# Kernel optimization log

Measured on AMD Instinct MI355X. Metric: run time of the kernel, lower is better.

Reference implementation:

```python
import jax, jax.numpy as jnp
import numpy as np

NUM_AGENTS = 5
B = 512          # graphs in batch
NP = 50          # nodes per graph
N = B * NP
EPG = 400        # edges per graph
E = B * EPG
H, C = 8, 64     # heads, per-head channels
F = H * C        # 512 node feature dim after concat
GRU_IN = 2 * F   # agent emb + graph emb
GRU_H = 128


def _gat_layer(x, src, dst, ea, W, a_src, a_dst, We, ae, b):
    # PyG GATConv: per-edge additive attention with edge features, softmax over dst
    n = x.shape[0]
    h = (x @ W).reshape(n, H, C)                          # [n,H,C]
    al = (h * a_src).sum(-1)[src] + (h * a_dst).sum(-1)[dst] \
         + ((ea @ We).reshape(-1, H, C) * ae).sum(-1)     # [e,H]
    al = jax.nn.leaky_relu(al, 0.2)
    amax = jax.ops.segment_max(al, dst, num_segments=n)
    amax = jnp.where(jnp.isfinite(amax), amax, 0.0)
    p = jnp.exp(al - amax[dst])
    denom = jax.ops.segment_sum(p, dst, num_segments=n)
    alpha = p / (denom[dst] + 1e-16)
    out = jax.ops.segment_sum(alpha[:, :, None] * h[src], dst, num_segments=n)
    return out.reshape(n, F) + b


def _gru(x_seq, h0, Wih, Whh, bih, bhh):
    # torch nn.GRU math, batch_first input [B,T,I]
    def step(h, x_t):
        gi = x_t @ Wih + bih
        gh = h @ Whh + bhh
        ir, iz, inn = jnp.split(gi, 3, axis=-1)
        hr, hz, hn = jnp.split(gh, 3, axis=-1)
        r = jax.nn.sigmoid(ir + hr)
        z = jax.nn.sigmoid(iz + hz)
        n_ = jnp.tanh(inn + r * hn)
        h_new = (1.0 - z) * n_ + z * h
        return h_new, h_new
    h_last, ys = jax.lax.scan(step, h0, jnp.swapaxes(x_seq, 0, 1))
    return jnp.swapaxes(ys, 0, 1), h_last


def _forward(x, edge_index, edge_attr, hidden_state,
             W1, a_src1, a_dst1, We1, ae1, b1,
             W2, a_src2, a_dst2, We2, ae2, b2,
             W3, a_src3, a_dst3, We3, ae3, b3,
             gru_Wih, gru_Whh, gru_bih, gru_bhh,
             fc1_W, fc1_b, fc2_W, fc2_b, log_std):
    src, dst = edge_index[0], edge_index[1]
    # conv1: add_self_loops=False
    x1 = jax.nn.relu(_gat_layer(x, src, dst, edge_attr, W1, a_src1, a_dst1, We1, ae1, b1))
    # conv2/3: add self loops with fill_value='mean' (mean of incoming edge_attr per node)
    cnt = jax.ops.segment_sum(jnp.ones((E,), x.dtype), dst, num_segments=N)
    loop_attr = jax.ops.segment_sum(edge_attr, dst, num_segments=N) / jnp.maximum(cnt, 1.0)[:, None]
    loops = jnp.arange(N, dtype=edge_index.dtype)
    src2 = jnp.concatenate([src, loops])
    dst2 = jnp.concatenate([dst, loops])
    ea2 = jnp.concatenate([edge_attr, loop_attr], axis=0)
    x2 = jax.nn.relu(_gat_layer(x1, src2, dst2, ea2, W2, a_src2, a_dst2, We2, ae2, b2))
    x3 = jax.nn.relu(_gat_layer(x2, src2, dst2, ea2, W3, a_src3, a_dst3, We3, ae3, b3))
    # global mean pool (each graph has NP nodes, contiguous)
    batch = jnp.repeat(jnp.arange(B), NP)
    graph_emb = jax.ops.segment_sum(x3, batch, num_segments=B) / NP   # [B,F]
    # first NUM_AGENTS nodes of each graph
    agent_idx = (jnp.arange(B)[:, None] * NP + jnp.arange(NUM_AGENTS)).reshape(-1)
    agent_emb = x3[agent_idx]                                          # [B*A,F]
    graph_rep = jnp.repeat(graph_emb, NUM_AGENTS, axis=0)
    combined = jnp.concatenate([agent_emb, graph_rep], axis=1).reshape(B, NUM_AGENTS, GRU_IN)
    gru_out, h_last = _gru(combined, hidden_state[0], gru_Wih, gru_Whh, gru_bih, gru_bhh)
    f1 = jax.nn.relu(gru_out.reshape(-1, GRU_H) @ fc1_W + fc1_b)
    action_mean = (f1 @ fc2_W + fc2_b).reshape(B, NUM_AGENTS, -1)
    action_std = jnp.broadcast_to(jnp.exp(jnp.clip(log_std, -20.0, 2.0)), action_mean.shape)
    return action_mean, action_std, h_last[None]


def setup_inputs() -> dict:
    ks = jax.random.split(jax.random.key(0), 24)
    rng = np.random.default_rng(0)
    # random edges within each graph, no self-loops
    src_l = rng.integers(0, NP, size=(B, EPG))
    dst_l = (src_l + 1 + rng.integers(0, NP - 1, size=(B, EPG))) % NP
    off = (np.arange(B) * NP)[:, None]
    edge_index = jnp.asarray(np.stack([(src_l + off).reshape(-1), (dst_l + off).reshape(-1)]), dtype=jnp.int32)

    def p(k, shape, fan):
        return jax.random.normal(k, shape, jnp.float32) / float(np.sqrt(fan))

    z = lambda *s: jnp.zeros(s, jnp.float32)
    return {
        "x": jax.random.normal(ks[0], (N, 4), jnp.float32),
        "edge_index": edge_index,
        "edge_attr": jax.random.uniform(ks[1], (E, 1), jnp.float32),
        "hidden_state": z(1, B, GRU_H),
        "W1": p(ks[2], (4, F), 4), "a_src1": p(ks[3], (H, C), C), "a_dst1": p(ks[4], (H, C), C),
        "We1": p(ks[5], (1, F), 1), "ae1": p(ks[6], (H, C), C), "b1": z(F),
        "W2": p(ks[7], (F, F), F), "a_src2": p(ks[8], (H, C), C), "a_dst2": p(ks[9], (H, C), C),
        "We2": p(ks[10], (1, F), 1), "ae2": p(ks[11], (H, C), C), "b2": z(F),
        "W3": p(ks[12], (F, F), F), "a_src3": p(ks[13], (H, C), C), "a_dst3": p(ks[14], (H, C), C),
        "We3": p(ks[15], (1, F), 1), "ae3": p(ks[16], (H, C), C), "b3": z(F),
        "gru_Wih": p(ks[17], (GRU_IN, 3 * GRU_H), GRU_IN),
        "gru_Whh": p(ks[18], (GRU_H, 3 * GRU_H), GRU_H),
        "gru_bih": z(3 * GRU_H), "gru_bhh": z(3 * GRU_H),
        "fc1_W": p(ks[19], (GRU_H, 64), GRU_H), "fc1_b": z(64),
        "fc2_W": p(ks[20], (64, 3), 64), "fc2_b": z(3),
        "log_std": jnp.full((1, 1, 3), -1.6, jnp.float32),
    }


def reference(x, edge_index, edge_attr, hidden_state,
              W1, a_src1, a_dst1, We1, ae1, b1,
              W2, a_src2, a_dst2, We2, ae2, b2,
              W3, a_src3, a_dst3, We3, ae3, b3,
              gru_Wih, gru_Whh, gru_bih, gru_bhh,
              fc1_W, fc1_b, fc2_W, fc2_b, log_std):
    return _forward(x, edge_index, edge_attr, hidden_state,
                    W1, a_src1, a_dst1, We1, ae1, b1,
                    W2, a_src2, a_dst2, We2, ae2, b2,
                    W3, a_src3, a_dst3, We3, ae3, b3,
                    gru_Wih, gru_Whh, gru_bih, gru_bhh,
                    fc1_W, fc1_b, fc2_W, fc2_b, log_std)
```

## Files before the change

kernel.cpp:

```cpp
#include <hip/hip_runtime.h>
#include <math.h>

#define NN 25600
#define BB 512
#define NP 50
#define EPG 400
#define EE 204800
#define HH 8
#define FF 512
#define GRUH 128
#define GRUIN 1024

typedef unsigned short ushort_t;
typedef __attribute__((ext_vector_type(8))) short bf16x8;
typedef __attribute__((ext_vector_type(4))) float f32x4;

__device__ __forceinline__ float wave_reduce_sum(float v) {
  #pragma unroll
  for (int m = 32; m >= 1; m >>= 1) v += __shfl_xor(v, m, 64);
  return v;
}

__device__ __forceinline__ ushort_t f2bf(float x) {
  union { float f; unsigned int u; } v; v.f = x;
  unsigned int r = v.u + 0x7fffu + ((v.u >> 16) & 1u);
  return (ushort_t)(r >> 16);
}

__device__ __forceinline__ float bf2f(ushort_t u) {
  union { unsigned int u; float f; } v; v.u = ((unsigned int)u) << 16;
  return v.f;
}

__device__ __forceinline__ void gload_lds16(const ushort_t* g, ushort_t* l) {
  __builtin_amdgcn_global_load_lds(
      (const __attribute__((address_space(1))) void*)g,
      (__attribute__((address_space(3))) void*)l, 16, 0, 0);
}

__global__ __launch_bounds__(256) void k_pre(
    const float* __restrict__ W2, const float* __restrict__ W3,
    const float* __restrict__ Wih,
    ushort_t* __restrict__ w2t, ushort_t* __restrict__ w3t, ushort_t* __restrict__ wiht,
    const int* __restrict__ ei, const float* __restrict__ eattr,
    int* __restrict__ rowp, ushort_t* __restrict__ esrc, float* __restrict__ eea,
    float* __restrict__ lattr,
    const float* __restrict__ We1, const float* __restrict__ ae1,
    const float* __restrict__ We2, const float* __restrict__ ae2,
    const float* __restrict__ We3, const float* __restrict__ ae3,
    float* __restrict__ wdot) {
  int b = blockIdx.x, tid = threadIdx.x;
  __shared__ float t[32][33];
  __shared__ int cnt[NP];
  __shared__ float esum[NP];
  __shared__ int rp[NP + 1];
  __shared__ int cur[NP];

  if (b < 896) {
    const float* W; ushort_t* Wt; int K, N, n0, k0;
    if (b < 256)      { W = W2;  Wt = w2t;  K = 512;  N = 512; n0 = (b & 15) * 32;        k0 = (b >> 4) * 32; }
    else if (b < 512) { W = W3;  Wt = w3t;  K = 512;  N = 512; n0 = ((b - 256) & 15) * 32; k0 = ((b - 256) >> 4) * 32; }
    else              { W = Wih; Wt = wiht; K = 1024; N = 384; n0 = ((b - 512) % 12) * 32; k0 = ((b - 512) / 12) * 32; }
    int tx = tid & 31, ty = tid >> 5;
    #pragma unroll
    for (int i = 0; i < 4; i++)
      t[ty + i * 8][tx] = W[(size_t)(k0 + ty + i * 8) * N + n0 + tx];
    __syncthreads();
    #pragma unroll
    for (int i = 0; i < 4; i++)
      Wt[(size_t)(n0 + ty + i * 8) * K + k0 + tx] = f2bf(t[tx][ty + i * 8]);
  } else if (b < 1408) {
    int g = b - 896;
    if (tid < NP) { cnt[tid] = 0; esum[tid] = 0.f; }
    __syncthreads();
    for (int e = tid; e < EPG; e += 256) {
      int ge = g * EPG + e;
      int dl = ei[EE + ge] - g * NP;
      atomicAdd(&cnt[dl], 1);
      atomicAdd(&esum[dl], eattr[ge]);
    }
    __syncthreads();
    if (tid == 0) {
      int s = 0;
      for (int i = 0; i < NP; i++) { rp[i] = s; cur[i] = s; s += cnt[i]; }
      rp[NP] = s;
    }
    __syncthreads();
    if (tid <= NP) rowp[g * 64 + tid] = rp[tid];
    if (tid < NP) lattr[g * NP + tid] = esum[tid] / (float)max(cnt[tid], 1);
    for (int e = tid; e < EPG; e += 256) {
      int ge = g * EPG + e;
      int sl = ei[ge] - g * NP;
      int dl = ei[EE + ge] - g * NP;
      int pos = atomicAdd(&cur[dl], 1);
      esrc[g * EPG + pos] = (ushort_t)sl;
      eea[g * EPG + pos] = eattr[ge];
    }
  } else {
    int w = tid >> 6, lane = tid & 63;
    for (int i = 0; i < 6; i++) {
      int idx = w + 4 * i;
      int l = idx >> 3, h = idx & 7;
      const float* We = l == 0 ? We1 : (l == 1 ? We2 : We3);
      const float* ae = l == 0 ? ae1 : (l == 1 ? ae2 : ae3);
      float v = wave_reduce_sum(We[h * 64 + lane] * ae[h * 64 + lane]);
      if (lane == 0) wdot[l * 8 + h] = v;
    }
  }
}

__global__ __launch_bounds__(256) void k_layer(
    const ushort_t* __restrict__ Xbf,
    const float* __restrict__ x4,
    const float* __restrict__ W1,
    const ushort_t* __restrict__ Wt,
    const float* __restrict__ a_src, const float* __restrict__ a_dst,
    ushort_t* __restrict__ xout,
    ushort_t* __restrict__ cbf,
    const int* __restrict__ rowp, const ushort_t* __restrict__ esrc,
    const float* __restrict__ eea, const float* __restrict__ lattr,
    const float* __restrict__ wdot_all, const float* __restrict__ bias,
    int layer, int self_loops) {
  int g = blockIdx.x, half = blockIdx.y, tid = threadIdx.x;
  int w = tid >> 6, l = tid & 63;
  int fbase = half * 256;
  int head = half * 4 + w;
  int m_l = l & 15, quad = l >> 4, rq = quad * 4, kq8 = quad * 8;

  __shared__ __align__(16) ushort_t hS[256 * 64];
  __shared__ __align__(16) ushort_t U[13696];
  __shared__ ushort_t esrcS[400];
  __shared__ float eeaS[400];
  __shared__ int rowpS[51];
  __shared__ float lattrS[50];
  __shared__ float sslS[256], sdlS[256];

  for (int i = tid; i < 400; i += 256) { esrcS[i] = esrc[g * EPG + i]; eeaS[i] = eea[g * EPG + i]; }
  if (tid <= NP) rowpS[tid] = rowp[g * 64 + tid];
  if (tid < NP) lattrS[tid] = lattr[g * NP + tid];

  f32x4 acc[4][4];
  #pragma unroll
  for (int i = 0; i < 4; i++)
    #pragma unroll
    for (int j = 0; j < 4; j++) acc[i][j] = (f32x4){0.f, 0.f, 0.f, 0.f};

  if (layer == 0) {
    float* W1s = (float*)U;
    float* xs = (float*)U + 1024;
    for (int i = tid; i < 1024; i += 256) {
      int k = i >> 8, j = i & 255;
      W1s[i] = W1[k * 512 + fbase + j];
    }
    if (tid < NP) *(float4*)(&xs[tid * 4]) = *(const float4*)(&x4[(size_t)(g * NP + tid) * 4]);
    else if (tid < 64) *(float4*)(&xs[tid * 4]) = make_float4(0.f, 0.f, 0.f, 0.f);
    __syncthreads();
    float xr[4][4];
    #pragma unroll
    for (int nt = 0; nt < 4; nt++)
      #pragma unroll
      for (int k = 0; k < 4; k++) xr[nt][k] = xs[(nt * 16 + m_l) * 4 + k];
    #pragma unroll
    for (int mt = 0; mt < 4; mt++) {
      float wv[4][4];
      #pragma unroll
      for (int r = 0; r < 4; r++)
        #pragma unroll
        for (int k = 0; k < 4; k++) wv[r][k] = W1s[k * 256 + w * 64 + mt * 16 + rq + r];
      #pragma unroll
      for (int nt = 0; nt < 4; nt++)
        #pragma unroll
        for (int r = 0; r < 4; r++)
          acc[mt][nt][r] = xr[nt][0] * wv[r][0] + xr[nt][1] * wv[r][1]
                         + xr[nt][2] * wv[r][2] + xr[nt][3] * wv[r][3];
    }
  } else {
    ushort_t* As = U;
    ushort_t* Bs = U + 8192;
    const ushort_t* Ag = Wt + (size_t)(fbase + w * 64 + (l >> 2)) * FF + (l & 3) * 8;
    const ushort_t* Bg = Xbf + (size_t)(g * NP + w * 16 + (l >> 2)) * FF + (l & 3) * 8;
    ushort_t* AsW = As + w * 2048;
    ushort_t* BsW = Bs + w * 512;
    for (int k0 = 0; k0 < FF; k0 += 32) {
      #pragma unroll
      for (int j = 0; j < 4; j++)
        gload_lds16(Ag + (size_t)j * 16 * FF + k0, AsW + j * 512);
      gload_lds16(Bg + k0, BsW);
      __syncthreads();
      bf16x8 af[4], bfr[4];
      #pragma unroll
      for (int mt = 0; mt < 4; mt++)
        af[mt] = *(const bf16x8*)(As + (w * 64 + mt * 16 + m_l) * 32 + kq8);
      #pragma unroll
      for (int nt = 0; nt < 4; nt++)
        bfr[nt] = *(const bf16x8*)(Bs + (nt * 16 + m_l) * 32 + kq8);
      #pragma unroll
      for (int mt = 0; mt < 4; mt++)
        #pragma unroll
        for (int nt = 0; nt < 4; nt++)
          acc[mt][nt] = __builtin_amdgcn_mfma_f32_16x16x32_bf16(af[mt], bfr[nt], acc[mt][nt], 0, 0, 0);
      __syncthreads();
    }
  }

  float ds[4] = {0.f, 0.f, 0.f, 0.f}, dd[4] = {0.f, 0.f, 0.f, 0.f};
  #pragma unroll
  for (int mt = 0; mt < 4; mt++) {
    float a_s[4], a_d[4];
    #pragma unroll
    for (int r = 0; r < 4; r++) {
      int fg = fbase + w * 64 + mt * 16 + rq + r;
      a_s[r] = a_src[fg]; a_d[r] = a_dst[fg];
    }
    #pragma unroll
    for (int nt = 0; nt < 4; nt++) {
      int s = nt * 16 + m_l;
      #pragma unroll
      for (int r = 0; r < 4; r++) {
        float v = acc[mt][nt][r];
        ds[nt] += v * a_s[r];
        dd[nt] += v * a_d[r];
        int fl = w * 64 + mt * 16 + rq + r;
        hS[fl * 64 + (s ^ ((fl & 3) << 3))] = f2bf(v);
      }
    }
  }
  #pragma unroll
  for (int nt = 0; nt < 4; nt++) {
    ds[nt] += __shfl_xor(ds[nt], 16, 64); ds[nt] += __shfl_xor(ds[nt], 32, 64);
    dd[nt] += __shfl_xor(dd[nt], 16, 64); dd[nt] += __shfl_xor(dd[nt], 32, 64);
  }
  if (l < 16) {
    #pragma unroll
    for (int nt = 0; nt < 4; nt++) {
      sslS[w * 64 + nt * 16 + l] = ds[nt];
      sdlS[w * 64 + nt * 16 + l] = dd[nt];
    }
  }
  __syncthreads();

  { uint4* z = (uint4*)U; for (int i = tid; i < 1712; i += 256) z[i] = make_uint4(0u, 0u, 0u, 0u); }
  __syncthreads();

  ushort_t* AmW = U + w * 3200;
  float wdot = wdot_all[layer * 8 + head];
  if (l < NP) {
    int d = l;
    int e0 = rowpS[d], e1 = rowpS[d + 1];
    float sd = sdlS[w * 64 + d];
    float m = -1e30f;
    for (int e = e0; e < e1; e++) {
      float al = sslS[w * 64 + esrcS[e]] + sd + eeaS[e] * wdot;
      al = al > 0.f ? al : 0.2f * al;
      m = fmaxf(m, al);
    }
    float al_loop = 0.f;
    if (self_loops) {
      al_loop = sslS[w * 64 + d] + sd + lattrS[d] * wdot;
      al_loop = al_loop > 0.f ? al_loop : 0.2f * al_loop;
      m = fmaxf(m, al_loop);
    }
    if (e1 > e0 || self_loops) {
      float denom = 0.f;
      for (int e = e0; e < e1; e++) {
        float al = sslS[w * 64 + esrcS[e]] + sd + eeaS[e] * wdot;
        al = al > 0.f ? al : 0.2f * al;
        float p = __expf(al - m);
        denom += p;
        int sp = esrcS[e] ^ ((d & 3) << 3);
        float prev = bf2f(AmW[d * 64 + sp]);
        AmW[d * 64 + sp] = f2bf(prev + p);
      }
      if (self_loops) {
        float p = __expf(al_loop - m);
        denom += p;
        int sp = d ^ ((d & 3) << 3);
        float prev = bf2f(AmW[d * 64 + sp]);
        AmW[d * 64 + sp] = f2bf(prev + p);
      }
      float inv = 1.f / (denom + 1e-16f);
      #pragma unroll
      for (int c = 0; c < 8; c++) {
        union { ushort_t u[8]; uint4 q; } pk;
        pk.q = *(uint4*)(AmW + d * 64 + c * 8);
        #pragma unroll
        for (int j = 0; j < 8; j++) pk.u[j] = f2bf(bf2f(pk.u[j]) * inv);
        *(uint4*)(AmW + d * 64 + c * 8) = pk.q;
      }
    }
  }
  __syncthreads();

  f32x4 oacc[4][4];
  #pragma unroll
  for (int i = 0; i < 4; i++)
    #pragma unroll
    for (int j = 0; j < 4; j++) oacc[i][j] = (f32x4){0.f, 0.f, 0.f, 0.f};
  #pragma unroll
  for (int kc = 0; kc < 2; kc++) {
    int kb = kc * 32 + kq8;
    bf16x8 bfr2[4];
    #pragma unroll
    for (int nt = 0; nt < 4; nt++) {
      int d = nt * 16 + m_l;
      bfr2[nt] = *(const bf16x8*)(AmW + d * 64 + (kb ^ ((d & 3) << 3)));
    }
    #pragma unroll
    for (int mt = 0; mt < 4; mt++) {
      int fl = w * 64 + mt * 16 + m_l;
      bf16x8 afr = *(const bf16x8*)(hS + fl * 64 + (kb ^ ((fl & 3) << 3)));
      #pragma unroll
      for (int nt = 0; nt < 4; nt++)
        oacc[mt][nt] = __builtin_amdgcn_mfma_f32_16x16x32_bf16(afr, bfr2[nt], oacc[mt][nt], 0, 0, 0);
    }
  }

  float vv[4][4][4];
  #pragma unroll
  for (int mt = 0; mt < 4; mt++) {
    const float4 bv = *(const float4*)(&bias[fbase + w * 64 + mt * 16 + rq]);
    #pragma unroll
    for (int nt = 0; nt < 4; nt++) {
      vv[mt][nt][0] = fmaxf(oacc[mt][nt][0] + bv.x, 0.f);
      vv[mt][nt][1] = fmaxf(oacc[mt][nt][1] + bv.y, 0.f);
      vv[mt][nt][2] = fmaxf(oacc[mt][nt][2] + bv.z, 0.f);
      vv[mt][nt][3] = fmaxf(oacc[mt][nt][3] + bv.w, 0.f);
    }
  }

  if (cbf == nullptr) {
    #pragma unroll
    for (int nt = 0; nt < 4; nt++) {
      int d = nt * 16 + m_l;
      if (d < NP) {
        #pragma unroll
        for (int mt = 0; mt < 4; mt++) {
          union { ushort_t u[4]; uint2 v; } pk;
          #pragma unroll
          for (int r = 0; r < 4; r++) pk.u[r] = f2bf(vv[mt][nt][r]);
          *(uint2*)(&xout[(size_t)(g * NP + d) * FF + fbase + w * 64 + mt * 16 + rq]) = pk.v;
        }
      }
    }
  } else {
    #pragma unroll
    for (int mt = 0; mt < 4; mt++) {
      float msum[4];
      #pragma unroll
      for (int r = 0; r < 4; r++) {
        float t = 0.f;
        #pragma unroll
        for (int nt = 0; nt < 4; nt++) {
          int d = nt * 16 + m_l;
          t += (d < NP) ? vv[mt][nt][r] : 0.f;
        }
        t += __shfl_xor(t, 1, 64); t += __shfl_xor(t, 2, 64);
        t += __shfl_xor(t, 4, 64); t += __shfl_xor(t, 8, 64);
        msum[r] = t * (1.f / NP);
      }
      if (m_l == 0) {
        union { ushort_t u[4]; uint2 v; } pk;
        #pragma unroll
        for (int r = 0; r < 4; r++) pk.u[r] = f2bf(msum[r]);
        #pragma unroll
        for (int t5 = 0; t5 < 5; t5++)
          *(uint2*)(&cbf[(size_t)(g * 5 + t5) * GRUIN + 512 + fbase + w * 64 + mt * 16 + rq]) = pk.v;
      }
      if (m_l < 5) {
        union { ushort_t u[4]; uint2 v; } pk;
        #pragma unroll
        for (int r = 0; r < 4; r++) pk.u[r] = f2bf(vv[mt][0][r]);
        *(uint2*)(&cbf[(size_t)(g * 5 + m_l) * GRUIN + fbase + w * 64 + mt * 16 + rq]) = pk.v;
      }
    }
  }
}

__global__ __launch_bounds__(256) void k_bgemm(
    const ushort_t* __restrict__ A, const ushort_t* __restrict__ Bt,
    const float* __restrict__ bias, float* __restrict__ C,
    int M, int N, int K) {
  __shared__ ushort_t As[128 * 32];
  __shared__ ushort_t Bs[128 * 32];
  int tid = threadIdx.x;
  int w = tid >> 6, l = tid & 63;
  int row0 = blockIdx.y * 128, col0 = blockIdx.x * 128;
  int wr = w >> 1, wc = w & 1;

  f32x4 acc[4][4];
  #pragma unroll
  for (int i = 0; i < 4; i++)
    #pragma unroll
    for (int j = 0; j < 4; j++) acc[i][j] = (f32x4){0.f, 0.f, 0.f, 0.f};

  int srow = w * 32 + (l >> 2);
  int skcol = (l & 3) * 8;
  const ushort_t* Ag = A + (size_t)(row0 + srow) * K + skcol;
  const ushort_t* Bg = Bt + (size_t)(col0 + srow) * K + skcol;
  ushort_t* AsW = &As[w * 1024];
  ushort_t* BsW = &Bs[w * 1024];

  int m_l = l & 15, kq = (l >> 4) * 8;
  const ushort_t* ArdA = &As[(wr * 64 + m_l) * 32 + kq];
  const ushort_t* BrdB = &Bs[(wc * 64 + m_l) * 32 + kq];

  for (int k0 = 0; k0 < K; k0 += 32) {
    gload_lds16(Ag + k0, AsW);
    gload_lds16(Ag + (size_t)16 * K + k0, AsW + 512);
    gload_lds16(Bg + k0, BsW);
    gload_lds16(Bg + (size_t)16 * K + k0, BsW + 512);
    __syncthreads();
    bf16x8 af[4], bfr[4];
    #pragma unroll
    for (int t = 0; t < 4; t++) {
      af[t]  = *(const bf16x8*)(ArdA + t * 16 * 32);
      bfr[t] = *(const bf16x8*)(BrdB + t * 16 * 32);
    }
    #pragma unroll
    for (int mt = 0; mt < 4; mt++)
      #pragma unroll
      for (int nt = 0; nt < 4; nt++)
        acc[mt][nt] = __builtin_amdgcn_mfma_f32_16x16x32_bf16(af[mt], bfr[nt], acc[mt][nt], 0, 0, 0);
    __syncthreads();
  }

  int cl = l & 15, rq = (l >> 4) * 4;
  #pragma unroll
  for (int mt = 0; mt < 4; mt++) {
    #pragma unroll
    for (int nt = 0; nt < 4; nt++) {
      int col = col0 + wc * 64 + nt * 16 + cl;
      float bv = bias ? bias[col] : 0.f;
      #pragma unroll
      for (int r = 0; r < 4; r++) {
        int row = row0 + wr * 64 + mt * 16 + rq + r;
        C[(size_t)row * N + col] = acc[mt][nt][r] + bv;
      }
    }
  }
}

__global__ void k_grufc(const float* __restrict__ gi_all, const float* __restrict__ h0,
                        const float* __restrict__ Whh, const float* __restrict__ bhh,
                        const float* __restrict__ fc1W, const float* __restrict__ fc1b,
                        const float* __restrict__ fc2W, const float* __restrict__ fc2b,
                        const float* __restrict__ log_std, float* __restrict__ dout) {
  int b = blockIdx.x, tid = threadIdx.x;
  __shared__ float hl[GRUH];
  __shared__ float ghb[384];
  __shared__ float go[5 * GRUH];
  __shared__ float f1[5 * 64];
  if (tid < GRUH) hl[tid] = h0[b * GRUH + tid];
  for (int t = 0; t < 5; t++) {
    __syncthreads();
    float acc = bhh[tid];
    for (int k = 0; k < GRUH; k++) acc += hl[k] * Whh[k * 384 + tid];
    ghb[tid] = acc;
    __syncthreads();
    if (tid < GRUH) {
      const float* gi = gi_all + (size_t)(b * 5 + t) * 384;
      float r = 1.f / (1.f + expf(-(gi[tid] + ghb[tid])));
      float z = 1.f / (1.f + expf(-(gi[128 + tid] + ghb[128 + tid])));
      float nn = tanhf(gi[256 + tid] + r * ghb[256 + tid]);
      float hn = (1.f - z) * nn + z * hl[tid];
      go[t * GRUH + tid] = hn;
      hl[tid] = hn;
    }
  }
  __syncthreads();
  if (tid < GRUH) dout[15360 + b * GRUH + tid] = hl[tid];
  if (tid < 320) {
    int t = tid >> 6, j = tid & 63;
    float acc = fc1b[j];
    for (int k = 0; k < GRUH; k++) acc += go[t * GRUH + k] * fc1W[k * 64 + j];
    f1[t * 64 + j] = fmaxf(acc, 0.f);
  }
  __syncthreads();
  if (tid < 15) {
    int t = tid / 3, o = tid % 3;
    float v = fc2b[o];
    for (int j = 0; j < 64; j++) v += f1[t * 64 + j] * fc2W[j * 3 + o];
    dout[(b * 5 + t) * 3 + o] = v;
    float ls = log_std[o];
    ls = fminf(fmaxf(ls, -20.f), 2.f);
    dout[7680 + (b * 5 + t) * 3 + o] = expf(ls);
  }
}

extern "C" void kernel_launch(void* const* d_in, const int* in_sizes, int n_in,
                              void* d_out, int out_size, void* d_ws, size_t ws_size,
                              hipStream_t stream) {
  const float* x      = (const float*)d_in[0];
  const int*   ei     = (const int*)d_in[1];
  const float* eattr  = (const float*)d_in[2];
  const float* hstate = (const float*)d_in[3];
  const float* W1  = (const float*)d_in[4];
  const float* as1 = (const float*)d_in[5];
  const float* ad1 = (const float*)d_in[6];
  const float* We1 = (const float*)d_in[7];
  const float* ae1 = (const float*)d_in[8];
  const float* b1  = (const float*)d_in[9];
  const float* W2  = (const float*)d_in[10];
  const float* as2 = (const float*)d_in[11];
  const float* ad2 = (const float*)d_in[12];
  const float* We2 = (const float*)d_in[13];
  const float* ae2 = (const float*)d_in[14];
  const float* b2  = (const float*)d_in[15];
  const float* W3  = (const float*)d_in[16];
  const float* as3 = (const float*)d_in[17];
  const float* ad3 = (const float*)d_in[18];
  const float* We3 = (const float*)d_in[19];
  const float* ae3 = (const float*)d_in[20];
  const float* b3  = (const float*)d_in[21];
  const float* Wih = (const float*)d_in[22];
  const float* Whh = (const float*)d_in[23];
  const float* bih = (const float*)d_in[24];
  const float* bhh = (const float*)d_in[25];
  const float* fc1W = (const float*)d_in[26];
  const float* fc1b = (const float*)d_in[27];
  const float* fc2W = (const float*)d_in[28];
  const float* fc2b = (const float*)d_in[29];
  const float* lstd = (const float*)d_in[30];

  float* ws = (float*)d_ws;
  ushort_t* xbf1 = (ushort_t*)ws;
  ushort_t* xbf2 = (ushort_t*)(ws + 6569984);
  float* p = ws + 2 * 6569984;
  int*   rowp  = (int*)p;         p += 32768;
  ushort_t* esrc = (ushort_t*)p;  p += 102400;
  float* eea   = p;               p += 204800;
  float* lattr = p;               p += 25600;
  float* wdot  = p;               p += 32;
  ushort_t* w2t  = (ushort_t*)p;  p += 131072;
  ushort_t* w3t  = (ushort_t*)p;  p += 131072;
  ushort_t* wiht = (ushort_t*)p;  p += 196608;
  ushort_t* cbf  = (ushort_t*)p;  p += 1310720;
  float* gi_all  = p;             p += 983040;
  float* dout = (float*)d_out;

  k_pre<<<1409, 256, 0, stream>>>(W2, W3, Wih, w2t, w3t, wiht, ei, eattr,
                                  rowp, esrc, eea, lattr,
                                  We1, ae1, We2, ae2, We3, ae3, wdot);

  k_layer<<<dim3(BB, 2), 256, 0, stream>>>(nullptr, x, W1, nullptr, as1, ad1,
                                           xbf1, nullptr, rowp, esrc, eea, lattr,
                                           wdot, b1, 0, 0);
  k_layer<<<dim3(BB, 2), 256, 0, stream>>>(xbf1, nullptr, nullptr, w2t, as2, ad2,
                                           xbf2, nullptr, rowp, esrc, eea, lattr,
                                           wdot, b2, 1, 1);
  k_layer<<<dim3(BB, 2), 256, 0, stream>>>(xbf2, nullptr, nullptr, w3t, as3, ad3,
                                           nullptr, cbf, rowp, esrc, eea, lattr,
                                           wdot, b3, 2, 1);

  k_bgemm<<<dim3(3, 20), 256, 0, stream>>>(cbf, wiht, bih, gi_all, 2560, 384, GRUIN);

  k_grufc<<<BB, 384, 0, stream>>>(gi_all, hstate, Whh, bhh, fc1W, fc1b,
                                  fc2W, fc2b, lstd, dout);
}
```

Before: 304.6 us.

## Split k_layer heads across 8 waves, load weight fragments directly from global

Doubles k_layer's block size to 512 threads so each head's 64 features are split across two waves, halving per-wave accumulators and raising occupancy. The weight operand is now read straight from global memory into registers instead of being staged in LDS. Node features are staged in larger 128-wide K chunks, so the loop syncs fewer times. Partial attention dot products from the two wave halves are combined through shared memory, and the hS swizzle and padded-row reads are adjusted. It risks more global traffic for weights that are no longer shared through LDS, and half the waves sit idle during the softmax phase.

```diff
diff --git a/kernel.cpp b/kernel.cpp
--- a/kernel.cpp
+++ b/kernel.cpp
@@ -109,49 +109,47 @@
   }
 }
 
-__global__ __launch_bounds__(256) void k_layer(
+__global__ __launch_bounds__(512, 4) void k_layer(
     const ushort_t* __restrict__ Xbf,
-    const float* __restrict__ x4,
-    const float* __restrict__ W1,
+    const float* __restrict__ x4, const float* __restrict__ W1,
     const ushort_t* __restrict__ Wt,
     const float* __restrict__ a_src, const float* __restrict__ a_dst,
-    ushort_t* __restrict__ xout,
-    ushort_t* __restrict__ cbf,
+    ushort_t* __restrict__ xout, ushort_t* __restrict__ cbf,
     const int* __restrict__ rowp, const ushort_t* __restrict__ esrc,
     const float* __restrict__ eea, const float* __restrict__ lattr,
     const float* __restrict__ wdot_all, const float* __restrict__ bias,
     int layer, int self_loops) {
   int g = blockIdx.x, half = blockIdx.y, tid = threadIdx.x;
   int w = tid >> 6, l = tid & 63;
+  int head = w & 3, fhalf = w >> 2;
+  int flb = head * 64 + fhalf * 32;
   int fbase = half * 256;
-  int head = half * 4 + w;
   int m_l = l & 15, quad = l >> 4, rq = quad * 4, kq8 = quad * 8;
 
   __shared__ __align__(16) ushort_t hS[256 * 64];
-  __shared__ __align__(16) ushort_t U[13696];
+  __shared__ __align__(16) ushort_t U[12800];
+  __shared__ float pds[512], pdd[512];
+  __shared__ float sslS[256], sdlS[256];
   __shared__ ushort_t esrcS[400];
   __shared__ float eeaS[400];
   __shared__ int rowpS[51];
   __shared__ float lattrS[50];
-  __shared__ float sslS[256], sdlS[256];
-
-  for (int i = tid; i < 400; i += 256) { esrcS[i] = esrc[g * EPG + i]; eeaS[i] = eea[g * EPG + i]; }
+
+  for (int i = tid; i < 400; i += 512) { esrcS[i] = esrc[g * EPG + i]; eeaS[i] = eea[g * EPG + i]; }
   if (tid <= NP) rowpS[tid] = rowp[g * 64 + tid];
   if (tid < NP) lattrS[tid] = lattr[g * NP + tid];
 
-  f32x4 acc[4][4];
-  #pragma unroll
-  for (int i = 0; i < 4; i++)
+  f32x4 acc[2][4];
+  #pragma unroll
+  for (int i = 0; i < 2; i++)
     #pragma unroll
     for (int j = 0; j < 4; j++) acc[i][j] = (f32x4){0.f, 0.f, 0.f, 0.f};
 
   if (layer == 0) {
     float* W1s = (float*)U;
     float* xs = (float*)U + 1024;
-    for (int i = tid; i < 1024; i += 256) {
-      int k = i >> 8, j = i & 255;
-      W1s[i] = W1[k * 512 + fbase + j];
-    }
+    for (int i = tid; i < 1024; i += 512)
+      W1s[i] = W1[(i >> 8) * 512 + fbase + (i & 255)];
     if (tid < NP) *(float4*)(&xs[tid * 4]) = *(const float4*)(&x4[(size_t)(g * NP + tid) * 4]);
     else if (tid < 64) *(float4*)(&xs[tid * 4]) = make_float4(0.f, 0.f, 0.f, 0.f);
     __syncthreads();
@@ -161,12 +159,12 @@
       #pragma unroll
       for (int k = 0; k < 4; k++) xr[nt][k] = xs[(nt * 16 + m_l) * 4 + k];
     #pragma unroll
-    for (int mt = 0; mt < 4; mt++) {
+    for (int mt = 0; mt < 2; mt++) {
       float wv[4][4];
       #pragma unroll
       for (int r = 0; r < 4; r++)
         #pragma unroll
-        for (int k = 0; k < 4; k++) wv[r][k] = W1s[k * 256 + w * 64 + mt * 16 + rq + r];
+        for (int k = 0; k < 4; k++) wv[r][k] = W1s[k * 256 + flb + mt * 16 + rq + r];
       #pragma unroll
       for (int nt = 0; nt < 4; nt++)
         #pragma unroll
@@ -174,42 +172,42 @@
           acc[mt][nt][r] = xr[nt][0] * wv[r][0] + xr[nt][1] * wv[r][1]
                          + xr[nt][2] * wv[r][2] + xr[nt][3] * wv[r][3];
     }
+    __syncthreads();
   } else {
-    ushort_t* As = U;
-    ushort_t* Bs = U + 8192;
-    const ushort_t* Ag = Wt + (size_t)(fbase + w * 64 + (l >> 2)) * FF + (l & 3) * 8;
+    ushort_t* Bs = U;
+    const ushort_t* Arow = Wt + (size_t)(fbase + flb + m_l) * FF + kq8;
     const ushort_t* Bg = Xbf + (size_t)(g * NP + w * 16 + (l >> 2)) * FF + (l & 3) * 8;
-    ushort_t* AsW = As + w * 2048;
-    ushort_t* BsW = Bs + w * 512;
-    for (int k0 = 0; k0 < FF; k0 += 32) {
-      #pragma unroll
-      for (int j = 0; j < 4; j++)
-        gload_lds16(Ag + (size_t)j * 16 * FF + k0, AsW + j * 512);
-      gload_lds16(Bg + k0, BsW);
+    ushort_t* BsW = U + w * 512;
+    for (int k0 = 0; k0 < FF; k0 += 128) {
+      if (w < 4) {
+        #pragma unroll
+        for (int j = 0; j < 4; j++)
+          gload_lds16(Bg + k0 + j * 32, BsW + j * 2048);
+      }
       __syncthreads();
-      bf16x8 af[4], bfr[4];
-      #pragma unroll
-      for (int mt = 0; mt < 4; mt++)
-        af[mt] = *(const bf16x8*)(As + (w * 64 + mt * 16 + m_l) * 32 + kq8);
-      #pragma unroll
-      for (int nt = 0; nt < 4; nt++)
-        bfr[nt] = *(const bf16x8*)(Bs + (nt * 16 + m_l) * 32 + kq8);
-      #pragma unroll
-      for (int mt = 0; mt < 4; mt++)
-        #pragma unroll
-        for (int nt = 0; nt < 4; nt++)
-          acc[mt][nt] = __builtin_amdgcn_mfma_f32_16x16x32_bf16(af[mt], bfr[nt], acc[mt][nt], 0, 0, 0);
+      #pragma unroll
+      for (int j = 0; j < 4; j++) {
+        int kk = k0 + j * 32;
+        bf16x8 af0 = *(const bf16x8*)(Arow + kk);
+        bf16x8 af1 = *(const bf16x8*)(Arow + (size_t)16 * FF + kk);
+        #pragma unroll
+        for (int nt = 0; nt < 4; nt++) {
+          bf16x8 bf = *(const bf16x8*)(Bs + j * 2048 + (nt * 16 + m_l) * 32 + kq8);
+          acc[0][nt] = __builtin_amdgcn_mfma_f32_16x16x32_bf16(af0, bf, acc[0][nt], 0, 0, 0);
+          acc[1][nt] = __builtin_amdgcn_mfma_f32_16x16x32_bf16(af1, bf, acc[1][nt], 0, 0, 0);
+        }
+      }
       __syncthreads();
     }
   }
 
   float ds[4] = {0.f, 0.f, 0.f, 0.f}, dd[4] = {0.f, 0.f, 0.f, 0.f};
   #pragma unroll
-  for (int mt = 0; mt < 4; mt++) {
+  for (int mt = 0; mt < 2; mt++) {
     float a_s[4], a_d[4];
     #pragma unroll
     for (int r = 0; r < 4; r++) {
-      int fg = fbase + w * 64 + mt * 16 + rq + r;
+      int fg = fbase + flb + mt * 16 + rq + r;
       a_s[r] = a_src[fg]; a_d[r] = a_dst[fg];
     }
     #pragma unroll
@@ -220,8 +218,8 @@
         float v = acc[mt][nt][r];
         ds[nt] += v * a_s[r];
         dd[nt] += v * a_d[r];
-        int fl = w * 64 + mt * 16 + rq + r;
-        hS[fl * 64 + (s ^ ((fl & 3) << 3))] = f2bf(v);
+        int fl = flb + mt * 16 + rq + r;
+        hS[fl * 64 + (s ^ (((fl >> 2) & 7) << 3))] = f2bf(v);
       }
     }
   }
@@ -233,18 +231,22 @@
   if (l < 16) {
     #pragma unroll
     for (int nt = 0; nt < 4; nt++) {
-      sslS[w * 64 + nt * 16 + l] = ds[nt];
-      sdlS[w * 64 + nt * 16 + l] = dd[nt];
+      pds[w * 64 + nt * 16 + l] = ds[nt];
+      pdd[w * 64 + nt * 16 + l] = dd[nt];
     }
   }
   __syncthreads();
 
-  { uint4* z = (uint4*)U; for (int i = tid; i < 1712; i += 256) z[i] = make_uint4(0u, 0u, 0u, 0u); }
+  { uint4* z = (uint4*)U; for (int i = tid; i < 1600; i += 512) z[i] = make_uint4(0u, 0u, 0u, 0u); }
+  if (tid < 256) {
+    sslS[tid] = pds[tid] + pds[tid + 256];
+    sdlS[tid] = pdd[tid] + pdd[tid + 256];
+  }
   __syncthreads();
 
-  ushort_t* AmW = U + w * 3200;
-  float wdot = wdot_all[layer * 8 + head];
-  if (l < NP) {
+  float wdot = wdot_all[layer * 8 + half * 4 + head];
+  if (w < 4 && l < NP) {
+    ushort_t* AmH = U + w * 3200;
     int d = l;
     int e0 = rowpS[d], e1 = rowpS[d + 1];
     float sd = sdlS[w * 64 + d];
@@ -268,32 +270,33 @@
         float p = __expf(al - m);
         denom += p;
         int sp = esrcS[e] ^ ((d & 3) << 3);
-        float prev = bf2f(AmW[d * 64 + sp]);
-        AmW[d * 64 + sp] = f2bf(prev + p);
+        float prev = bf2f(AmH[d * 64 + sp]);
+        AmH[d * 64 + sp] = f2bf(prev + p);
       }
       if (self_loops) {
         float p = __expf(al_loop - m);
         denom += p;
         int sp = d ^ ((d & 3) << 3);
-        float prev = bf2f(AmW[d * 64 + sp]);
-        AmW[d * 64 + sp] = f2bf(prev + p);
+        float prev = bf2f(AmH[d * 64 + sp]);
+        AmH[d * 64 + sp] = f2bf(prev + p);
       }
       float inv = 1.f / (denom + 1e-16f);
       #pragma unroll
       for (int c = 0; c < 8; c++) {
         union { ushort_t u[8]; uint4 q; } pk;
-        pk.q = *(uint4*)(AmW + d * 64 + c * 8);
+        pk.q = *(uint4*)(AmH + d * 64 + c * 8);
         #pragma unroll
         for (int j = 0; j < 8; j++) pk.u[j] = f2bf(bf2f(pk.u[j]) * inv);
-        *(uint4*)(AmW + d * 64 + c * 8) = pk.q;
+        *(uint4*)(AmH + d * 64 + c * 8) = pk.q;
       }
     }
   }
   __syncthreads();
 
-  f32x4 oacc[4][4];
-  #pragma unroll
-  for (int i = 0; i < 4; i++)
+  ushort_t* AmW = U + head * 3200;
+  f32x4 oacc[2][4];
+  #pragma unroll
+  for (int i = 0; i < 2; i++)
     #pragma unroll
     for (int j = 0; j < 4; j++) oacc[i][j] = (f32x4){0.f, 0.f, 0.f, 0.f};
   #pragma unroll
@@ -303,22 +306,23 @@
     #pragma unroll
     for (int nt = 0; nt < 4; nt++) {
       int d = nt * 16 + m_l;
-      bfr2[nt] = *(const bf16x8*)(AmW + d * 64 + (kb ^ ((d & 3) << 3)));
-    }
-    #pragma unroll
-    for (int mt = 0; mt < 4; mt++) {
-      int fl = w * 64 + mt * 16 + m_l;
-      bf16x8 afr = *(const bf16x8*)(hS + fl * 64 + (kb ^ ((fl & 3) << 3)));
+      int rd = d < NP ? d : 0;
+      bfr2[nt] = *(const bf16x8*)(AmW + rd * 64 + (kb ^ ((rd & 3) << 3)));
+    }
+    #pragma unroll
+    for (int mt = 0; mt < 2; mt++) {
+      int fl = flb + mt * 16 + m_l;
+      bf16x8 afr = *(const bf16x8*)(hS + fl * 64 + (kb ^ (((fl >> 2) & 7) << 3)));
       #pragma unroll
       for (int nt = 0; nt < 4; nt++)
         oacc[mt][nt] = __builtin_amdgcn_mfma_f32_16x16x32_bf16(afr, bfr2[nt], oacc[mt][nt], 0, 0, 0);
     }
   }
 
-  float vv[4][4][4];
-  #pragma unroll
-  for (int mt = 0; mt < 4; mt++) {
-    const float4 bv = *(const float4*)(&bias[fbase + w * 64 + mt * 16 + rq]);
+  float vv[2][4][4];
+  #pragma unroll
+  for (int mt = 0; mt < 2; mt++) {
+    const float4 bv = *(const float4*)(&bias[fbase + flb + mt * 16 + rq]);
     #pragma unroll
     for (int nt = 0; nt < 4; nt++) {
       vv[mt][nt][0] = fmaxf(oacc[mt][nt][0] + bv.x, 0.f);
@@ -334,17 +338,17 @@
       int d = nt * 16 + m_l;
       if (d < NP) {
         #pragma unroll
-        for (int mt = 0; mt < 4; mt++) {
+        for (int mt = 0; mt < 2; mt++) {
           union { ushort_t u[4]; uint2 v; } pk;
           #pragma unroll
           for (int r = 0; r < 4; r++) pk.u[r] = f2bf(vv[mt][nt][r]);
-          *(uint2*)(&xout[(size_t)(g * NP + d) * FF + fbase + w * 64 + mt * 16 + rq]) = pk.v;
+          *(uint2*)(&xout[(size_t)(g * NP + d) * FF + fbase + flb + mt * 16 + rq]) = pk.v;
         }
       }
     }
   } else {
     #pragma unroll
-    for (int mt = 0; mt < 4; mt++) {
+    for (int mt = 0; mt < 2; mt++) {
       float msum[4];
       #pragma unroll
       for (int r = 0; r < 4; r++) {
@@ -364,13 +368,13 @@
         for (int r = 0; r < 4; r++) pk.u[r] = f2bf(msum[r]);
         #pragma unroll
         for (int t5 = 0; t5 < 5; t5++)
-          *(uint2*)(&cbf[(size_t)(g * 5 + t5) * GRUIN + 512 + fbase + w * 64 + mt * 16 + rq]) = pk.v;
+          *(uint2*)(&cbf[(size_t)(g * 5 + t5) * GRUIN + 512 + fbase + flb + mt * 16 + rq]) = pk.v;
       }
       if (m_l < 5) {
         union { ushort_t u[4]; uint2 v; } pk;
         #pragma unroll
         for (int r = 0; r < 4; r++) pk.u[r] = f2bf(vv[mt][0][r]);
-        *(uint2*)(&cbf[(size_t)(g * 5 + m_l) * GRUIN + fbase + w * 64 + mt * 16 + rq]) = pk.v;
+        *(uint2*)(&cbf[(size_t)(g * 5 + m_l) * GRUIN + fbase + flb + mt * 16 + rq]) = pk.v;
       }
     }
   }
@@ -542,13 +546,13 @@
                                   rowp, esrc, eea, lattr,
                                   We1, ae1, We2, ae2, We3, ae3, wdot);
 
-  k_layer<<<dim3(BB, 2), 256, 0, stream>>>(nullptr, x, W1, nullptr, as1, ad1,
+  k_layer<<<dim3(BB, 2), 512, 0, stream>>>(nullptr, x, W1, nullptr, as1, ad1,
                                            xbf1, nullptr, rowp, esrc, eea, lattr,
                                            wdot, b1, 0, 0);
-  k_layer<<<dim3(BB, 2), 256, 0, stream>>>(xbf1, nullptr, nullptr, w2t, as2, ad2,
+  k_layer<<<dim3(BB, 2), 512, 0, stream>>>(xbf1, nullptr, nullptr, w2t, as2, ad2,
                                            xbf2, nullptr, rowp, esrc, eea, lattr,
                                            wdot, b2, 1, 1);
-  k_layer<<<dim3(BB, 2), 256, 0, stream>>>(xbf2, nullptr, nullptr, w3t, as3, ad3,
+  k_layer<<<dim3(BB, 2), 512, 0, stream>>>(xbf2, nullptr, nullptr, w3t, as3, ad3,
                                            nullptr, cbf, rowp, esrc, eea, lattr,
                                            wdot, b3, 2, 1);
 
```

After: 318.8 us. 1.05x slower.
